# Optimization experiments

Measured on AMD Instinct MI355X. Metric: run time of the kernel, lower is better.

The kernel has to match this reference:

```python
import jax, jax.numpy as jnp
import numpy as np

EMBED_DIM = 1024
B, S = 4, 4096


def setup_inputs() -> dict:
    key = jax.random.key(0)
    kx, kq, kk, kv = jax.random.split(key, 4)
    x = jax.random.normal(kx, (B, S, EMBED_DIM), dtype=jnp.float32)
    W_Q = jax.random.normal(kq, (EMBED_DIM, EMBED_DIM), dtype=jnp.float32)
    W_K = jax.random.normal(kk, (EMBED_DIM, EMBED_DIM), dtype=jnp.float32)
    W_V = jax.random.normal(kv, (EMBED_DIM, EMBED_DIM), dtype=jnp.float32)
    return {"x": x, "W_Q": W_Q, "W_K": W_K, "W_V": W_V}


def reference(x, W_Q, W_K, W_V):
    # Q, K, V: [B, S, D]
    Q = x @ W_Q
    K = x @ W_K
    V = x @ W_V
    scale = 1.0 / jnp.sqrt(jnp.float32(EMBED_DIM))
    # scores: [B, S, S] (full score matrix, as in the original)
    scores = jnp.einsum('bsd,btd->bst', Q, K) * scale
    attn = jax.nn.softmax(scores, axis=-1)
    # output: [B, S, D]
    Z = jnp.einsum('bst,btd->bsd', attn, V)
    return Z
```

## Files before the change

### kernel.cpp

```cpp
#include <hip/hip_runtime.h>


typedef _Float16 half8 __attribute__((ext_vector_type(8)));
typedef _Float16 half4v __attribute__((ext_vector_type(4)));
typedef float floatx4 __attribute__((ext_vector_type(4)));

__device__ __forceinline__ void glds16(const _Float16* g, _Float16* l) {
    __builtin_amdgcn_global_load_lds(
        (const __attribute__((address_space(1))) void*)g,
        (__attribute__((address_space(3))) void*)l, 16, 0, 0);
}

template <bool SPLITIN, int OMODE, bool PMAX>
__global__ __launch_bounds__(256, 2) void gemm_nt(
    const _Float16* __restrict__ AH, const _Float16* __restrict__ AL,
    const _Float16* BH, const _Float16* BL,
    void* out0, void* out1,
    const float* __restrict__ rdiv, float* __restrict__ pmax,
    float scale, int M, int N, int K,
    const _Float16* BH2, const _Float16* BL2, void* o0b, void* o1b)
{
    if (blockIdx.z == 1) { BH = BH2; BL = BL2; out0 = o0b; out1 = o1b; }

    __shared__ _Float16 sAH[2 * 128 * 32];
    __shared__ _Float16 sBH[2 * 128 * 32];
    __shared__ _Float16 sAL[SPLITIN ? 2 * 128 * 32 : 8];
    __shared__ _Float16 sBL[SPLITIN ? 2 * 128 * 32 : 8];

    const int tid = threadIdx.x;
    const int bm = blockIdx.y, bn = blockIdx.x;
    const int lane = tid & 63, quad = lane >> 4, lrow = lane & 15;
    const int wave = tid >> 6, wm = wave >> 1, wn = wave & 1;

    const int wb = (tid & 192) * 8;
    const size_t g0 = (size_t)(tid >> 2) * K + (tid & 3) * 8;
    const size_t g1 = (size_t)((256 + tid) >> 2) * K + (tid & 3) * 8;
    const _Float16* pA0 = AH + (size_t)bm * 128 * K + g0;
    const _Float16* pA1 = AH + (size_t)bm * 128 * K + g1;
    const _Float16* pB0 = BH + (size_t)bn * 128 * K + g0;
    const _Float16* pB1 = BH + (size_t)bn * 128 * K + g1;
    const _Float16* pA0L = SPLITIN ? (AL + (size_t)bm * 128 * K + g0) : nullptr;
    const _Float16* pA1L = SPLITIN ? (AL + (size_t)bm * 128 * K + g1) : nullptr;
    const _Float16* pB0L = SPLITIN ? (BL + (size_t)bn * 128 * K + g0) : nullptr;
    const _Float16* pB1L = SPLITIN ? (BL + (size_t)bn * 128 * K + g1) : nullptr;

    floatx4 acc[4][4] = {};

    const int aoff = (wm * 64 + lrow) * 32 + quad * 8;
    const int boff = (wn * 64 + lrow) * 32 + quad * 8;

    glds16(pA0, sAH + wb);        glds16(pA1, sAH + 2048 + wb);
    glds16(pB0, sBH + wb);        glds16(pB1, sBH + 2048 + wb);
    if (SPLITIN) {
        glds16(pA0L, sAL + wb);   glds16(pA1L, sAL + 2048 + wb);
        glds16(pB0L, sBL + wb);   glds16(pB1L, sBL + 2048 + wb);
    }
    pA0 += 32; pA1 += 32; pB0 += 32; pB1 += 32;
    if (SPLITIN) { pA0L += 32; pA1L += 32; pB0L += 32; pB1L += 32; }

    int cur = 0;
    for (int k0 = 0; k0 < K; k0 += 32) {
        __syncthreads();

        if (k0 + 32 < K) {
            const int nb = (cur ^ 1) * 4096;
            glds16(pA0, sAH + nb + wb);        glds16(pA1, sAH + nb + 2048 + wb);
            glds16(pB0, sBH + nb + wb);        glds16(pB1, sBH + nb + 2048 + wb);
            if (SPLITIN) {
                glds16(pA0L, sAL + nb + wb);   glds16(pA1L, sAL + nb + 2048 + wb);
                glds16(pB0L, sBL + nb + wb);   glds16(pB1L, sBL + nb + 2048 + wb);
            }
            pA0 += 32; pA1 += 32; pB0 += 32; pB1 += 32;
            if (SPLITIN) { pA0L += 32; pA1L += 32; pB0L += 32; pB1L += 32; }
        }

        const int cb = cur * 4096;
        half8 aH[4], bH[4], aL[4], bL[4];
        #pragma unroll
        for (int i = 0; i < 4; ++i) {
            aH[i] = *(const half8*)&sAH[cb + aoff + i * 16 * 32];
            bH[i] = *(const half8*)&sBH[cb + boff + i * 16 * 32];
            if (SPLITIN) {
                aL[i] = *(const half8*)&sAL[cb + aoff + i * 16 * 32];
                bL[i] = *(const half8*)&sBL[cb + boff + i * 16 * 32];
            }
        }
        #pragma unroll
        for (int mi = 0; mi < 4; ++mi)
            #pragma unroll
            for (int nj = 0; nj < 4; ++nj) {
                acc[mi][nj] = __builtin_amdgcn_mfma_f32_16x16x32_f16(
                    aH[mi], bH[nj], acc[mi][nj], 0, 0, 0);
                if (SPLITIN) {
                    acc[mi][nj] = __builtin_amdgcn_mfma_f32_16x16x32_f16(
                        aH[mi], bL[nj], acc[mi][nj], 0, 0, 0);
                    acc[mi][nj] = __builtin_amdgcn_mfma_f32_16x16x32_f16(
                        aL[mi], bH[nj], acc[mi][nj], 0, 0, 0);
                }
            }
        cur ^= 1;
    }

    #pragma unroll
    for (int mi = 0; mi < 4; ++mi) {
        #pragma unroll
        for (int r = 0; r < 4; ++r) {
            const int grow = bm * 128 + wm * 64 + mi * 16 + quad * 4 + r;
            float s = scale;
            if (OMODE == 1) s = scale / rdiv[grow];
            float v[4];
            #pragma unroll
            for (int nj = 0; nj < 4; ++nj) v[nj] = acc[mi][nj][r] * s;
            if (PMAX) {
                float mx = fmaxf(fmaxf(v[0], v[1]), fmaxf(v[2], v[3]));
                #pragma unroll
                for (int off = 1; off < 16; off <<= 1)
                    mx = fmaxf(mx, __shfl_xor(mx, off));
                if (lrow == 0) pmax[(size_t)grow * 64 + bn * 2 + wn] = mx;
            }
            #pragma unroll
            for (int nj = 0; nj < 4; ++nj) {
                const int gcol = bn * 128 + wn * 64 + nj * 16 + lrow;
                const size_t idx = (size_t)grow * N + gcol;
                if (OMODE <= 1) {
                    ((float*)out0)[idx] = v[nj];
                } else if (OMODE == 2) {
                    ((_Float16*)out0)[idx] = (_Float16)v[nj];
                } else {
                    const _Float16 h = (_Float16)v[nj];
                    ((_Float16*)out0)[idx] = h;
                    ((_Float16*)out1)[idx] = (_Float16)(v[nj] - (float)h);
                }
            }
        }
    }
}

__global__ __launch_bounds__(256) void split_scale(
    const float* __restrict__ x, _Float16* __restrict__ hi,
    _Float16* __restrict__ lo, int n)
{
    int i = (blockIdx.x * 256 + threadIdx.x) * 4;
    const int stride = gridDim.x * 256 * 4;
    for (; i < n; i += stride) {
        float4 v = *(const float4*)(x + i);
        float a[4] = {v.x * 256.f, v.y * 256.f, v.z * 256.f, v.w * 256.f};
        half4v h, l;
        #pragma unroll
        for (int j = 0; j < 4; ++j) {
            h[j] = (_Float16)a[j];
            l[j] = (_Float16)(a[j] - (float)h[j]);
        }
        *(half4v*)(hi + i) = h;
        *(half4v*)(lo + i) = l;
    }
}

__global__ __launch_bounds__(256) void wprep3(
    const float* __restrict__ W0, const float* __restrict__ W1,
    const float* __restrict__ W2,
    _Float16* __restrict__ h0, _Float16* __restrict__ l0,
    _Float16* __restrict__ h1, _Float16* __restrict__ l1,
    _Float16* __restrict__ h2, int dim)
{
    const int z = blockIdx.z;
    const float* W = (z == 0) ? W0 : (z == 1) ? W1 : W2;
    _Float16* hiT = (z == 0) ? h0 : (z == 1) ? h1 : h2;
    _Float16* loT = (z == 0) ? l0 : (z == 1) ? l1 : nullptr;

    __shared__ float t[32][33];
    const int n0 = blockIdx.x * 32, k0 = blockIdx.y * 32;
    const int tx = threadIdx.x, ty = threadIdx.y;
    #pragma unroll
    for (int i = 0; i < 4; ++i)
        t[ty + 8 * i][tx] = 256.f * W[(size_t)(k0 + ty + 8 * i) * dim + n0 + tx];
    __syncthreads();
    #pragma unroll
    for (int i = 0; i < 4; ++i) {
        const int nn = ty + 8 * i;
        const float v = t[tx][nn];
        const _Float16 h = (_Float16)v;
        const size_t o = (size_t)(n0 + nn) * dim + k0 + tx;
        hiT[o] = h;
        if (loT) loT[o] = (_Float16)(v - (float)h);
    }
}

__global__ __launch_bounds__(256) void softmax_p(
    const float* __restrict__ Sc, const float* __restrict__ pmax,
    _Float16* __restrict__ P, float* __restrict__ rowsum)
{
    __shared__ float red[8];
    const int tid = threadIdx.x;
    const int row = blockIdx.x;
    const float* srow = Sc + (size_t)row * 4096;
    _Float16* prow = P + (size_t)row * 4096;

    if (tid < 64) {
        float m = pmax[(size_t)row * 64 + tid];
        #pragma unroll
        for (int off = 32; off; off >>= 1) m = fmaxf(m, __shfl_xor(m, off));
        if (tid == 0) red[0] = m;
    }
    __syncthreads();
    const float rmax = red[0];

    float s = 0.f;
    for (int c = tid * 4; c < 4096; c += 1024) {
        float4 v = *(const float4*)(srow + c);
        float p0 = __expf(v.x - rmax), p1 = __expf(v.y - rmax);
        float p2 = __expf(v.z - rmax), p3 = __expf(v.w - rmax);
        s += p0 + p1 + p2 + p3;
        half4v h = {(_Float16)p0, (_Float16)p1, (_Float16)p2, (_Float16)p3};
        *(half4v*)(prow + c) = h;
    }
    #pragma unroll
    for (int off = 32; off; off >>= 1) s += __shfl_xor(s, off, 64);
    if ((tid & 63) == 0) red[4 + (tid >> 6)] = s;
    __syncthreads();
    if (tid == 0) rowsum[row] = red[4] + red[5] + red[6] + red[7];
}

extern "C" void kernel_launch(void* const* d_in, const int* in_sizes, int n_in,
                              void* d_out, int out_size, void* d_ws, size_t ws_size,
                              hipStream_t stream) {
    const int Bb = 4, S = 4096, D = 1024;
    const size_t SD = (size_t)S * D;
    const size_t SS = (size_t)S * S;

    const float* x  = (const float*)d_in[0];
    const float* WQ = (const float*)d_in[1];
    const float* WK = (const float*)d_in[2];
    const float* WV = (const float*)d_in[3];
    float* out = (float*)d_out;

    char* w = (char*)d_ws;
    _Float16* WQhT = (_Float16*)w;  w += (size_t)D * D * 2;
    _Float16* WQlT = (_Float16*)w;  w += (size_t)D * D * 2;
    _Float16* WKhT = (_Float16*)w;  w += (size_t)D * D * 2;
    _Float16* WKlT = (_Float16*)w;  w += (size_t)D * D * 2;
    _Float16* WvhT = (_Float16*)w;  w += (size_t)D * D * 2;
    _Float16* xhi  = (_Float16*)w;  w += SD * 2;
    _Float16* xlo  = (_Float16*)w;  w += SD * 2;
    _Float16* Qhi  = (_Float16*)w;  w += SD * 2;
    _Float16* Qlo  = (_Float16*)w;  w += SD * 2;
    _Float16* Khi  = (_Float16*)w;  w += SD * 2;
    _Float16* Klo  = (_Float16*)w;  w += SD * 2;
    _Float16* VT   = (_Float16*)w;  w += SD * 2;
    float*    rowsum = (float*)w;   w += (size_t)S * 4;
    float*    pmax = (float*)w;     w += (size_t)S * 64 * 4;
    float*    Sc   = (float*)w;     w += SS * 4;
    _Float16* P    = (_Float16*)w;  w += SS * 2;

    const float kInv256 = 0.00390625f;
    const float kScScale = 4.76837158203125e-7f;

    dim3 blk(256);

    wprep3<<<dim3(32, 32, 3), dim3(32, 8), 0, stream>>>(
        WQ, WK, WV, WQhT, WQlT, WKhT, WKlT, WvhT, D);

    for (int b = 0; b < Bb; ++b) {
        const float* xb = x + (size_t)b * SD;
        float* outb = out + (size_t)b * SD;

        split_scale<<<dim3(4096), blk, 0, stream>>>(xb, xhi, xlo, (int)SD);

        gemm_nt<true, 3, false><<<dim3(D / 128, S / 128, 2), blk, 0, stream>>>(
            xhi, xlo, WQhT, WQlT, Qhi, Qlo, nullptr, nullptr, kInv256, S, D, D,
            WKhT, WKlT, Khi, Klo);

        gemm_nt<false, 2, false><<<dim3(S / 128, D / 128, 1), blk, 0, stream>>>(
            WvhT, nullptr, xhi, nullptr, VT, nullptr, nullptr, nullptr, kInv256,
            D, S, D, nullptr, nullptr, nullptr, nullptr);

        gemm_nt<true, 0, true><<<dim3(S / 128, S / 128, 1), blk, 0, stream>>>(
            Qhi, Qlo, Khi, Klo, Sc, nullptr, nullptr, pmax, kScScale, S, S, D,
            nullptr, nullptr, nullptr, nullptr);

        softmax_p<<<dim3(S), blk, 0, stream>>>(Sc, pmax, P, rowsum);

        gemm_nt<false, 1, false><<<dim3(D / 128, S / 128, 1), blk, 0, stream>>>(
            P, nullptr, VT, nullptr, outb, nullptr, rowsum, nullptr, kInv256,
            S, D, S, nullptr, nullptr, nullptr, nullptr);
    }
}
```

Before: 1.268 ms.

## Add dedicated 256x256 QK^T kernel with phased LDS pipelining

```diff
diff --git a/kernel.cpp b/kernel.cpp
--- a/kernel.cpp
+++ b/kernel.cpp
@@ -10,6 +10,144 @@
         (const __attribute__((address_space(1))) void*)g,
         (__attribute__((address_space(3))) void*)l, 16, 0, 0);
 }
+
+
+struct QKTD { const _Float16* a; const _Float16* b; int ko; };
+
+#define QK_VM(n) asm volatile("s_waitcnt vmcnt(" #n ")" ::: "memory")
+#define QK_NOP ((void)0)
+
+#define QK_PHASE(BUF, Q, STAGES, WAITS)                                         \
+    do {                                                                        \
+        if ((Q) == 0) {                                                         \
+            _Pragma("unroll") for (int mi = 0; mi < 4; ++mi) {                  \
+                af[mi][0] = *(const half8*)&sA[(BUF)*16384 + (abase + mi*16)*64 + s0]; \
+                af[mi][1] = *(const half8*)&sA[(BUF)*16384 + (abase + mi*16)*64 + s1]; \
+            }                                                                   \
+        }                                                                       \
+        half8 bf[2][2];                                                         \
+        _Pragma("unroll") for (int nj = 0; nj < 2; ++nj) {                      \
+            bf[nj][0] = *(const half8*)&sB[(BUF)*16384 + (bbase + (Q)*32 + nj*16)*64 + s0]; \
+            bf[nj][1] = *(const half8*)&sB[(BUF)*16384 + (bbase + (Q)*32 + nj*16)*64 + s1]; \
+        }                                                                       \
+        STAGES;                                                                 \
+        __builtin_amdgcn_sched_barrier(0);           \
+        __builtin_amdgcn_s_barrier();                                           \
+        asm volatile("s_waitcnt lgkmcnt(0)" ::: "memory");                      \
+        __builtin_amdgcn_sched_barrier(0);                                      \
+        __builtin_amdgcn_s_setprio(1);                                          \
+        _Pragma("unroll") for (int mi = 0; mi < 4; ++mi)                        \
+            _Pragma("unroll") for (int nj = 0; nj < 2; ++nj) {                  \
+                acc[mi][(Q)*2 + nj] = __builtin_amdgcn_mfma_f32_16x16x32_f16(   \
+                    af[mi][0], bf[nj][0], acc[mi][(Q)*2 + nj], 0, 0, 0);        \
+                acc[mi][(Q)*2 + nj] = __builtin_amdgcn_mfma_f32_16x16x32_f16(   \
+                    af[mi][1], bf[nj][1], acc[mi][(Q)*2 + nj], 0, 0, 0);        \
+            }                                                                   \
+        __builtin_amdgcn_s_setprio(0);                                          \
+        WAITS;                                                                  \
+        __builtin_amdgcn_s_barrier();                                           \
+        __builtin_amdgcn_sched_barrier(0);                                      \
+    } while (0)
+
+__global__ __launch_bounds__(512, 2) void qk8(
+    const _Float16* __restrict__ QH, const _Float16* __restrict__ QL,
+    const _Float16* __restrict__ KH, const _Float16* __restrict__ KL,
+    float* __restrict__ Sc, float* __restrict__ pmax, float scale)
+{
+    __shared__ _Float16 sA[2 * 256 * 64];
+    __shared__ _Float16 sB[2 * 256 * 64];
+
+    const int tid = threadIdx.x;
+    const int bm = blockIdx.y, bn = blockIdx.x;
+    const int lane = tid & 63, w = tid >> 6;
+    const int quad = lane >> 4, lrow = lane & 15;
+    const int wm = w >> 1, wn = w & 1;
+    const int sx = lrow & 7;
+    const int s0 = (quad ^ sx) * 8;
+    const int s1 = s0 ^ 32;
+    const int abase = wm * 64 + lrow;
+    const int bbase = wn * 128 + lrow;
+    const int wbase = w * 512;
+
+    const int srow = tid >> 3;
+    const int scol = ((tid & 7) ^ (srow & 7)) * 8;
+    const size_t ga = (size_t)(bm * 256 + srow) * 1024 + scol;
+    const size_t gb = (size_t)(bn * 256 + srow) * 1024 + scol;
+
+    floatx4 acc[4][8] = {};
+    half8 af[4][2];
+
+    auto td = [&](int t) {
+        const int d = t / 3, m = t - d * 3;
+        return QKTD{m == 2 ? QL : QH, m == 1 ? KL : KH, d * 64};
+    };
+    auto stageA4 = [&](int b, QKTD s) {
+        const _Float16* g = s.a + ga + s.ko;
+        _Float16* l = sA + b * 16384 + wbase;
+        glds16(g, l);
+        glds16(g + 64 * 1024, l + 4096);
+        glds16(g + 128 * 1024, l + 8192);
+        glds16(g + 192 * 1024, l + 12288);
+    };
+    auto stageBq = [&](int b, int qr, QKTD s) {
+        glds16(s.b + gb + (size_t)(qr * 64) * 1024 + s.ko,
+               sB + b * 16384 + qr * 4096 + wbase);
+    };
+
+    {
+        QKTD t0 = td(0), t1 = td(1);
+        stageA4(0, t0);
+        stageBq(0, 0, t0); stageBq(0, 2, t0);
+        stageBq(0, 1, t0); stageBq(0, 3, t0);
+        stageA4(1, t1);
+        stageBq(1, 0, t1); stageBq(1, 2, t1);
+    }
+    __builtin_amdgcn_sched_barrier(0);
+    QK_VM(6);
+    __builtin_amdgcn_s_barrier();
+    __builtin_amdgcn_sched_barrier(0);
+
+    #pragma unroll 1
+    for (int i = 0; i < 24; ++i) {
+        const int i2 = 2 * i + 2 < 47 ? 2 * i + 2 : 47;
+        const int i3 = 2 * i + 3 < 47 ? 2 * i + 3 : 47;
+        const QKTD t1 = td(2 * i + 1);
+        const QKTD ta = td(i2);
+        const QKTD tb = td(i3);
+        QK_PHASE(0, 0, { stageBq(1, 1, t1); stageBq(1, 3, t1); }, QK_NOP);
+        QK_PHASE(0, 1, stageA4(0, ta), QK_VM(12));
+        QK_PHASE(0, 2, { stageBq(0, 0, ta); stageBq(0, 2, ta); }, QK_NOP);
+        QK_PHASE(0, 3, QK_NOP, QK_VM(8));
+        QK_PHASE(1, 0, { stageBq(0, 1, ta); stageBq(0, 3, ta); }, QK_NOP);
+        QK_PHASE(1, 1, stageA4(1, tb), QK_VM(12));
+        QK_PHASE(1, 2, { stageBq(1, 0, tb); stageBq(1, 2, tb); }, QK_NOP);
+        QK_PHASE(1, 3, QK_NOP, QK_VM(8));
+    }
+
+    QK_VM(0);
+    __builtin_amdgcn_sched_barrier(0);
+
+    #pragma unroll
+    for (int mi = 0; mi < 4; ++mi) {
+        #pragma unroll
+        for (int r = 0; r < 4; ++r) {
+            const int grow = bm * 256 + wm * 64 + mi * 16 + quad * 4 + r;
+            float v[8];
+            #pragma unroll
+            for (int nc = 0; nc < 8; ++nc) v[nc] = acc[mi][nc][r] * scale;
+            float mx = fmaxf(fmaxf(fmaxf(v[0], v[1]), fmaxf(v[2], v[3])),
+                             fmaxf(fmaxf(v[4], v[5]), fmaxf(v[6], v[7])));
+            #pragma unroll
+            for (int off = 1; off < 16; off <<= 1)
+                mx = fmaxf(mx, __shfl_xor(mx, off));
+            if (lrow == 0) pmax[(size_t)grow * 32 + bn * 2 + wn] = mx;
+            float* so = Sc + (size_t)grow * 4096 + bn * 256 + wn * 128;
+            #pragma unroll
+            for (int nc = 0; nc < 8; ++nc) so[nc * 16 + lrow] = v[nc];
+        }
+    }
+}
+
 
 template <bool SPLITIN, int OMODE, bool PMAX>
 __global__ __launch_bounds__(256, 2) void gemm_nt(
@@ -196,10 +334,10 @@
     const float* srow = Sc + (size_t)row * 4096;
     _Float16* prow = P + (size_t)row * 4096;
 
-    if (tid < 64) {
-        float m = pmax[(size_t)row * 64 + tid];
-        #pragma unroll
-        for (int off = 32; off; off >>= 1) m = fmaxf(m, __shfl_xor(m, off));
+    if (tid < 32) {
+        float m = pmax[(size_t)row * 32 + tid];
+        #pragma unroll
+        for (int off = 16; off; off >>= 1) m = fmaxf(m, __shfl_xor(m, off));
         if (tid == 0) red[0] = m;
     }
     __syncthreads();
@@ -274,9 +412,8 @@
             WvhT, nullptr, xhi, nullptr, VT, nullptr, nullptr, nullptr, kInv256,
             D, S, D, nullptr, nullptr, nullptr, nullptr);
 
-        gemm_nt<true, 0, true><<<dim3(S / 128, S / 128, 1), blk, 0, stream>>>(
-            Qhi, Qlo, Khi, Klo, Sc, nullptr, nullptr, pmax, kScScale, S, S, D,
-            nullptr, nullptr, nullptr, nullptr);
+        qk8<<<dim3(S / 256, S / 256), dim3(512), 0, stream>>>(
+            Qhi, Qlo, Khi, Klo, Sc, pmax, kScScale);
 
         softmax_p<<<dim3(S), blk, 0, stream>>>(Sc, pmax, P, rowsum);
 
```

New measurement: 1.196 ms. 1.06x faster.

## Add dedicated 256x256-tile QK^T kernel with 8 waves for split-fp16 scores

Applied to the files above, without the earlier changes.

```diff
diff --git a/kernel.cpp b/kernel.cpp
--- a/kernel.cpp
+++ b/kernel.cpp
@@ -10,6 +10,107 @@
         (const __attribute__((address_space(1))) void*)g,
         (__attribute__((address_space(3))) void*)l, 16, 0, 0);
 }
+
+
+__global__ __launch_bounds__(512, 2) void qk8(
+    const _Float16* __restrict__ QH, const _Float16* __restrict__ QL,
+    const _Float16* __restrict__ KH, const _Float16* __restrict__ KL,
+    float* __restrict__ Sc, float* __restrict__ pmax, float scale)
+{
+    __shared__ _Float16 sP[2 * 32768];
+
+    const int tid = threadIdx.x;
+    const int bm = blockIdx.y, bn = blockIdx.x;
+    const int lane = tid & 63, w = tid >> 6;
+    const int quad = lane >> 4, lrow = lane & 15;
+    const int wm = w >> 1, wn = w & 1;
+
+    const int s0h = ((((lrow & 1) << 2) + quad) ^ ((lrow >> 1) & 7)) * 8;
+    const int arow2 = wm * 32 + (lrow >> 1);
+    const int brow2 = wn * 64 + (lrow >> 1);
+
+    const int sp = (tid & 7) ^ ((tid >> 3) & 7);
+    const int gR = 2 * (tid >> 3) + (sp >> 2);
+    const int gk = (sp & 3) * 8;
+    const size_t ga = (size_t)(bm * 256 + gR) * 1024 + gk;
+    const size_t gb = (size_t)(bn * 256 + gR) * 1024 + gk;
+
+    floatx4 acc[4][8] = {};
+
+    auto stageAll = [&](int b, int ko) {
+        _Float16* l = sP + b * 32768 + tid * 8;
+        glds16(QH + ga + ko, l);
+        glds16(QH + ga + ko + 131072, l + 4096);
+        glds16(QL + ga + ko, l + 8192);
+        glds16(QL + ga + ko + 131072, l + 12288);
+        glds16(KH + gb + ko, l + 16384);
+        glds16(KH + gb + ko + 131072, l + 20480);
+        glds16(KL + gb + ko, l + 24576);
+        glds16(KL + gb + ko + 131072, l + 28672);
+    };
+
+    stageAll(0, 0);
+
+    #pragma unroll 1
+    for (int c = 0; c < 32; ++c) {
+        __syncthreads();
+
+        if (c < 31) stageAll((c + 1) & 1, (c + 1) * 32);
+
+        const int cb = (c & 1) * 32768;
+        half8 aH[4], aL[4];
+        #pragma unroll
+        for (int mi = 0; mi < 4; ++mi) {
+            aH[mi] = *(const half8*)&sP[cb + (arow2 + mi * 8) * 64 + s0h];
+            aL[mi] = *(const half8*)&sP[cb + 8192 + (arow2 + mi * 8) * 64 + s0h];
+        }
+        #pragma unroll
+        for (int q = 0; q < 4; ++q) {
+            half8 bh[2], bl[2];
+            #pragma unroll
+            for (int nj = 0; nj < 2; ++nj) {
+                bh[nj] = *(const half8*)&sP[cb + 16384 + (brow2 + q * 16 + nj * 8) * 64 + s0h];
+                bl[nj] = *(const half8*)&sP[cb + 24576 + (brow2 + q * 16 + nj * 8) * 64 + s0h];
+            }
+            __builtin_amdgcn_s_setprio(1);
+            #pragma unroll
+            for (int mi = 0; mi < 4; ++mi)
+                #pragma unroll
+                for (int nj = 0; nj < 2; ++nj) {
+                    acc[mi][q * 2 + nj] = __builtin_amdgcn_mfma_f32_16x16x32_f16(
+                        aH[mi], bh[nj], acc[mi][q * 2 + nj], 0, 0, 0);
+                    acc[mi][q * 2 + nj] = __builtin_amdgcn_mfma_f32_16x16x32_f16(
+                        aH[mi], bl[nj], acc[mi][q * 2 + nj], 0, 0, 0);
+                    acc[mi][q * 2 + nj] = __builtin_amdgcn_mfma_f32_16x16x32_f16(
+                        aL[mi], bh[nj], acc[mi][q * 2 + nj], 0, 0, 0);
+                }
+            __builtin_amdgcn_s_setprio(0);
+        }
+    }
+
+    asm volatile("s_waitcnt vmcnt(0) lgkmcnt(0)" ::: "memory");
+
+    #pragma unroll
+    for (int mi = 0; mi < 4; ++mi) {
+        #pragma unroll
+        for (int r = 0; r < 4; ++r) {
+            const int grow = bm * 256 + wm * 64 + mi * 16 + quad * 4 + r;
+            float v[8];
+            #pragma unroll
+            for (int nc = 0; nc < 8; ++nc) v[nc] = acc[mi][nc][r] * scale;
+            float mx = fmaxf(fmaxf(fmaxf(v[0], v[1]), fmaxf(v[2], v[3])),
+                             fmaxf(fmaxf(v[4], v[5]), fmaxf(v[6], v[7])));
+            #pragma unroll
+            for (int off = 1; off < 16; off <<= 1)
+                mx = fmaxf(mx, __shfl_xor(mx, off));
+            if (lrow == 0) pmax[(size_t)grow * 32 + bn * 2 + wn] = mx;
+            float* so = Sc + (size_t)grow * 4096 + bn * 256 + wn * 128;
+            #pragma unroll
+            for (int nc = 0; nc < 8; ++nc) so[nc * 16 + lrow] = v[nc];
+        }
+    }
+}
+
 
 template <bool SPLITIN, int OMODE, bool PMAX>
 __global__ __launch_bounds__(256, 2) void gemm_nt(
@@ -196,10 +297,10 @@
     const float* srow = Sc + (size_t)row * 4096;
     _Float16* prow = P + (size_t)row * 4096;
 
-    if (tid < 64) {
-        float m = pmax[(size_t)row * 64 + tid];
-        #pragma unroll
-        for (int off = 32; off; off >>= 1) m = fmaxf(m, __shfl_xor(m, off));
+    if (tid < 32) {
+        float m = pmax[(size_t)row * 32 + tid];
+        #pragma unroll
+        for (int off = 16; off; off >>= 1) m = fmaxf(m, __shfl_xor(m, off));
         if (tid == 0) red[0] = m;
     }
     __syncthreads();
@@ -274,9 +375,8 @@
             WvhT, nullptr, xhi, nullptr, VT, nullptr, nullptr, nullptr, kInv256,
             D, S, D, nullptr, nullptr, nullptr, nullptr);
 
-        gemm_nt<true, 0, true><<<dim3(S / 128, S / 128, 1), blk, 0, stream>>>(
-            Qhi, Qlo, Khi, Klo, Sc, nullptr, nullptr, pmax, kScScale, S, S, D,
-            nullptr, nullptr, nullptr, nullptr);
+        qk8<<<dim3(S / 256, S / 256), dim3(512), 0, stream>>>(
+            Qhi, Qlo, Khi, Klo, Sc, pmax, kScScale);
 
         softmax_p<<<dim3(S), blk, 0, stream>>>(Sc, pmax, P, rowsum);
 
```

After: 1.164 ms. 8.2% less time.
